# Kernel tuning notes

Measured on AMD Instinct MI355X. Metric: run time of the kernel, lower is better.

Reference implementation:

```python
import jax, jax.numpy as jnp
import numpy as np

B, S, HLEN, VLEN, HID = 32, 2048, 1024, 1024, 1024


def setup_inputs() -> dict:
    key = jax.random.key(0)
    ks = jax.random.split(key, 6)
    scale_W = 1.0 / np.sqrt(HLEN)
    scale_U = 1.0 / np.sqrt(VLEN)
    scale_w = 1.0 / np.sqrt(HID)
    return {
        "h": jax.random.normal(ks[0], (B, HLEN), dtype=jnp.float32),
        "V": jax.random.normal(ks[1], (B, S, VLEN), dtype=jnp.float32),
        "W_w": jax.random.normal(ks[2], (HID, HLEN), dtype=jnp.float32) * scale_W,
        "W_b": jax.random.normal(ks[3], (HID,), dtype=jnp.float32) * scale_W,
        "U_w": jax.random.normal(ks[4], (HID, VLEN), dtype=jnp.float32) * scale_U,
        "w_w": jax.random.normal(ks[5], (HID,), dtype=jnp.float32) * scale_w,
    }


def reference(h, V, W_w, W_b, U_w, w_w):
    # e = w^T tanh(W h + U V^T + b); beta = softmax(e); out = sum_s beta_s V_s
    h_proj = h @ W_w.T + W_b                      # [B, HID]
    V_proj = jnp.einsum('bsv,dv->bsd', V, U_w)    # [B, S, HID]
    e = jnp.einsum('bsd,d->bs', jnp.tanh(h_proj[:, None, :] + V_proj), w_w)  # [B, S]
    beta = jax.nn.softmax(e, axis=1)              # [B, S]
    return jnp.einsum('bs,bsv->bv', beta, V)      # [B, VLEN]
```

## Files before the change

### kernel.cpp

```cpp
#include <hip/hip_runtime.h>

constexpr int B_   = 32;
constexpr int S_   = 2048;
constexpr int HID_ = 1024;
constexpr int VL_  = 1024;

typedef __attribute__((ext_vector_type(4))) float  f32x4;
typedef __attribute__((ext_vector_type(4))) short  s16x4;
typedef __attribute__((ext_vector_type(8))) short  s16x8;

__device__ __forceinline__ short f2bf(float f) {
    union { float f; unsigned u; } v; v.f = f;
    unsigned r = v.u + 0x7fffu + ((v.u >> 16) & 1u);
    return (short)(r >> 16);
}

__device__ __forceinline__ float bf2f(short s) {
    union { unsigned u; float f; } v;
    v.u = ((unsigned)(unsigned short)s) << 16;
    return v.f;
}

__device__ __forceinline__ float fast_tanh(float x) {
    float e2 = __expf(2.0f * x);
    return 1.0f - 2.0f / (e2 + 1.0f);
}

__device__ __forceinline__ void async_cp16(const void* g, void* l) {
    __builtin_amdgcn_global_load_lds(
        (const __attribute__((address_space(1))) unsigned int*)g,
        (__attribute__((address_space(3))) unsigned int*)l,
        16, 0, 0);
}

__global__ __launch_bounds__(256) void hproj_kernel(const float* __restrict__ h,
                                                    const float* __restrict__ Ww,
                                                    const float* __restrict__ Wb,
                                                    float* __restrict__ hp) {
    int tid = threadIdx.x;
    int wave = tid >> 6, lane = tid & 63;
    int d = blockIdx.x * 4 + wave;
    const float* wr = Ww + (size_t)d * HID_;
    float4 wreg[4];
#pragma unroll
    for (int i = 0; i < 4; i++) wreg[i] = *(const float4*)(wr + i * 256 + lane * 4);
    float bias = Wb[d];
    for (int b = 0; b < B_; b++) {
        const float* hr = h + (size_t)b * HID_;
        float acc = 0.0f;
#pragma unroll
        for (int i = 0; i < 4; i++) {
            float4 x = *(const float4*)(hr + i * 256 + lane * 4);
            acc += wreg[i].x * x.x + wreg[i].y * x.y + wreg[i].z * x.z + wreg[i].w * x.w;
        }
#pragma unroll
        for (int o = 32; o; o >>= 1) acc += __shfl_xor(acc, o);
        if (lane == 0) hp[(size_t)b * HID_ + d] = acc + bias;
    }
}

__global__ __launch_bounds__(256) void cvt_kernel(const float* __restrict__ src,
                                                  short* __restrict__ dst, size_t n4) {
    size_t i = (size_t)blockIdx.x * blockDim.x + threadIdx.x;
    size_t stride = (size_t)gridDim.x * blockDim.x;
    for (; i < n4; i += stride) {
        float4 x = ((const float4*)src)[i];
        s16x4 y;
        y.x = f2bf(x.x); y.y = f2bf(x.y); y.z = f2bf(x.z); y.w = f2bf(x.w);
        ((s16x4*)dst)[i] = y;
    }
}

__global__ __launch_bounds__(256) void e_kernel_bf16(const short* __restrict__ Vm,
                                                     const short* __restrict__ Um,
                                                     const float* __restrict__ hp,
                                                     const float* __restrict__ ww,
                                                     float* __restrict__ epart) {
    __shared__ short As[128][32];
    __shared__ short Bs[128][32];
    __shared__ float ebuf[2][128];

    int tid = threadIdx.x;
    int dh = blockIdx.x;
    int s0 = blockIdx.y * 128;
    int b  = blockIdx.z;
    int wave = tid >> 6, lane = tid & 63;
    int wm = wave >> 1, wn = wave & 1;
    int col = lane & 15, quad = lane >> 4;

    int r0 = 32 * wave + (lane >> 2);
    int kc = (lane & 3) * 8;
    const short* gAb = Vm + ((size_t)b * S_ + s0 + r0) * VL_ + kc;
    short* lA0 = &As[32 * wave][0];
    short* lA1 = &As[32 * wave + 16][0];
    short* lB0 = &Bs[32 * wave][0];
    short* lB1 = &Bs[32 * wave + 16][0];

    float ep[4][4];
#pragma unroll
    for (int i = 0; i < 4; i++)
#pragma unroll
        for (int j = 0; j < 4; j++) ep[i][j] = 0.0f;

    for (int dt = dh * 4; dt < dh * 4 + 4; dt++) {
        int d0 = dt * 128;
        const short* gA0 = gAb;
        const short* gA1 = gAb + 16 * (size_t)VL_;
        const short* gB0 = Um + ((size_t)d0 + r0) * VL_ + kc;
        const short* gB1 = gB0 + 16 * (size_t)VL_;

        f32x4 zero = {0.f, 0.f, 0.f, 0.f};
        f32x4 acc[4][4];
#pragma unroll
        for (int i = 0; i < 4; i++)
#pragma unroll
            for (int j = 0; j < 4; j++) acc[i][j] = zero;

        for (int k0 = 0; k0 < VL_; k0 += 32) {
            async_cp16(gA0, lA0);
            async_cp16(gA1, lA1);
            async_cp16(gB0, lB0);
            async_cp16(gB1, lB1);
            gA0 += 32; gA1 += 32; gB0 += 32; gB1 += 32;
            __syncthreads();

            s16x8 a8[4], b8[4];
#pragma unroll
            for (int tm = 0; tm < 4; tm++)
                a8[tm] = *(const s16x8*)&As[wm * 64 + tm * 16 + col][quad * 8];
#pragma unroll
            for (int tn = 0; tn < 4; tn++)
                b8[tn] = *(const s16x8*)&Bs[wn * 64 + tn * 16 + col][quad * 8];
#pragma unroll
            for (int tm = 0; tm < 4; tm++)
#pragma unroll
                for (int tn = 0; tn < 4; tn++)
                    acc[tm][tn] = __builtin_amdgcn_mfma_f32_16x16x32_bf16(
                        a8[tm], b8[tn], acc[tm][tn], 0, 0, 0);
            __syncthreads();
        }

        float wv[4], hv[4];
#pragma unroll
        for (int tn = 0; tn < 4; tn++) {
            int d = d0 + wn * 64 + tn * 16 + col;
            wv[tn] = ww[d];
            hv[tn] = hp[(size_t)b * HID_ + d];
        }
#pragma unroll
        for (int tm = 0; tm < 4; tm++)
#pragma unroll
            for (int reg = 0; reg < 4; reg++) {
#pragma unroll
                for (int tn = 0; tn < 4; tn++)
                    ep[tm][reg] += wv[tn] * fast_tanh(hv[tn] + acc[tm][tn][reg]);
            }
    }

#pragma unroll
    for (int tm = 0; tm < 4; tm++)
#pragma unroll
        for (int reg = 0; reg < 4; reg++) {
            float p = ep[tm][reg];
            p += __shfl_xor(p, 1);
            p += __shfl_xor(p, 2);
            p += __shfl_xor(p, 4);
            p += __shfl_xor(p, 8);
            if (col == 0)
                ebuf[wn][wm * 64 + tm * 16 + quad * 4 + reg] = p;
        }
    __syncthreads();
    if (tid < 128)
        epart[((size_t)dh * B_ + b) * S_ + s0 + tid] = ebuf[0][tid] + ebuf[1][tid];
}

__global__ __launch_bounds__(256) void e_kernel_f32(const float* __restrict__ Vm,
                                                    const float* __restrict__ Um,
                                                    const float* __restrict__ hp,
                                                    const float* __restrict__ ww,
                                                    float* __restrict__ e) {
    __shared__ short As[128][40];
    __shared__ short Bs[128][40];
    int tid = threadIdx.x;
    int b  = blockIdx.z;
    int d0 = blockIdx.x * 128;
    int s0 = blockIdx.y * 128;
    int wave = tid >> 6, lane = tid & 63;
    int wm = wave >> 1, wn = wave & 1;
    int col = lane & 15, quad = lane >> 4;

    f32x4 zero = {0.f, 0.f, 0.f, 0.f};
    f32x4 acc[4][4];
#pragma unroll
    for (int i = 0; i < 4; i++)
#pragma unroll
        for (int j = 0; j < 4; j++) acc[i][j] = zero;

    const float* Abase = Vm + ((size_t)b * S_ + s0) * (size_t)VL_;
    const float* Bbase = Um + (size_t)d0 * (size_t)VL_;

    for (int k0 = 0; k0 < VL_; k0 += 32) {
        int k4 = tid & 7, rb = tid >> 3;
#pragma unroll
        for (int i = 0; i < 4; i++) {
            int r = rb + 32 * i;
            float4 x = *(const float4*)(Abase + (size_t)r * VL_ + k0 + k4 * 4);
            s16x4 ya; ya.x = f2bf(x.x); ya.y = f2bf(x.y); ya.z = f2bf(x.z); ya.w = f2bf(x.w);
            *(s16x4*)&As[r][k4 * 4] = ya;
            float4 y = *(const float4*)(Bbase + (size_t)r * VL_ + k0 + k4 * 4);
            s16x4 yb; yb.x = f2bf(y.x); yb.y = f2bf(y.y); yb.z = f2bf(y.z); yb.w = f2bf(y.w);
            *(s16x4*)&Bs[r][k4 * 4] = yb;
        }
        __syncthreads();
        s16x8 a8[4], b8[4];
#pragma unroll
        for (int tm = 0; tm < 4; tm++)
            a8[tm] = *(const s16x8*)&As[wm * 64 + tm * 16 + col][quad * 8];
#pragma unroll
        for (int tn = 0; tn < 4; tn++)
            b8[tn] = *(const s16x8*)&Bs[wn * 64 + tn * 16 + col][quad * 8];
#pragma unroll
        for (int tm = 0; tm < 4; tm++)
#pragma unroll
            for (int tn = 0; tn < 4; tn++)
                acc[tm][tn] = __builtin_amdgcn_mfma_f32_16x16x32_bf16(
                    a8[tm], b8[tn], acc[tm][tn], 0, 0, 0);
        __syncthreads();
    }

    float wv[4], hv[4];
#pragma unroll
    for (int tn = 0; tn < 4; tn++) {
        int d = d0 + wn * 64 + tn * 16 + col;
        wv[tn] = ww[d];
        hv[tn] = hp[(size_t)b * HID_ + d];
    }
#pragma unroll
    for (int tm = 0; tm < 4; tm++) {
#pragma unroll
        for (int reg = 0; reg < 4; reg++) {
            float p = 0.0f;
#pragma unroll
            for (int tn = 0; tn < 4; tn++)
                p += wv[tn] * fast_tanh(hv[tn] + acc[tm][tn][reg]);
            p += __shfl_xor(p, 1);
            p += __shfl_xor(p, 2);
            p += __shfl_xor(p, 4);
            p += __shfl_xor(p, 8);
            if (col == 0) {
                int s = s0 + wm * 64 + tm * 16 + quad * 4 + reg;
                atomicAdd(&e[(size_t)b * S_ + s], p);
            }
        }
    }
}

__global__ __launch_bounds__(256) void softmax_kernel(const float* __restrict__ epart,
                                                      float* __restrict__ beta,
                                                      int nparts) {
    int b = blockIdx.x, tid = threadIdx.x;
    const float* r0 = epart + (size_t)b * S_;
    const float* r1 = epart + ((size_t)B_ + b) * S_;
    float v[8];
    float m = -1e30f;
#pragma unroll
    for (int i = 0; i < 8; i++) {
        int idx = tid + i * 256;
        v[i] = r0[idx] + (nparts > 1 ? r1[idx] : 0.0f);
        m = fmaxf(m, v[i]);
    }
#pragma unroll
    for (int o = 32; o; o >>= 1) m = fmaxf(m, __shfl_xor(m, o));
    __shared__ float rm[4], rs[4];
    int wave = tid >> 6, lane = tid & 63;
    if (lane == 0) rm[wave] = m;
    __syncthreads();
    m = fmaxf(fmaxf(rm[0], rm[1]), fmaxf(rm[2], rm[3]));
    float s = 0.0f;
#pragma unroll
    for (int i = 0; i < 8; i++) { v[i] = __expf(v[i] - m); s += v[i]; }
#pragma unroll
    for (int o = 32; o; o >>= 1) s += __shfl_xor(s, o);
    if (lane == 0) rs[wave] = s;
    __syncthreads();
    s = rs[0] + rs[1] + rs[2] + rs[3];
    float inv = 1.0f / s;
#pragma unroll
    for (int i = 0; i < 8; i++) beta[(size_t)b * S_ + tid + i * 256] = v[i] * inv;
}

__global__ __launch_bounds__(256) void out_kernel_bf16(const float* __restrict__ beta,
                                                       const short* __restrict__ Vb16,
                                                       float* __restrict__ opart) {
    int b = blockIdx.x, sc = blockIdx.y;
    int v4 = threadIdx.x;
    const short* Vp = Vb16 + ((size_t)b * S_ + (size_t)sc * 128) * VL_;
    const float* bb = beta + (size_t)b * S_ + (size_t)sc * 128;
    float ax = 0.f, ay = 0.f, az = 0.f, aw = 0.f;
    for (int s = 0; s < 128; s++) {
        float w = bb[s];
        s16x4 x = *(const s16x4*)(Vp + (size_t)s * VL_ + v4 * 4);
        ax += w * bf2f(x.x); ay += w * bf2f(x.y);
        az += w * bf2f(x.z); aw += w * bf2f(x.w);
    }
    float4 r = {ax, ay, az, aw};
    *(float4*)(opart + (((size_t)b * 16 + sc) * VL_) + v4 * 4) = r;
}

__global__ __launch_bounds__(256) void out_reduce_kernel(const float* __restrict__ opart,
                                                         float* __restrict__ out) {
    int b = blockIdx.x, v4 = threadIdx.x;
    float4 a = {0.f, 0.f, 0.f, 0.f};
    const float* base = opart + (size_t)b * 16 * VL_;
#pragma unroll
    for (int sc = 0; sc < 16; sc++) {
        float4 x = *(const float4*)(base + (size_t)sc * VL_ + v4 * 4);
        a.x += x.x; a.y += x.y; a.z += x.z; a.w += x.w;
    }
    *(float4*)(out + (size_t)b * VL_ + v4 * 4) = a;
}

__global__ __launch_bounds__(256) void out_kernel_f32(const float* __restrict__ beta,
                                                      const float* __restrict__ V,
                                                      float* __restrict__ out) {
    int b = blockIdx.x, sc = blockIdx.y;
    int v4 = threadIdx.x;
    const float* Vb = V + ((size_t)b * S_ + (size_t)sc * 128) * VL_;
    const float* bb = beta + (size_t)b * S_ + (size_t)sc * 128;
    float ax = 0.f, ay = 0.f, az = 0.f, aw = 0.f;
    for (int s = 0; s < 128; s++) {
        float w = bb[s];
        float4 x = *(const float4*)(Vb + (size_t)s * VL_ + v4 * 4);
        ax += w * x.x; ay += w * x.y; az += w * x.z; aw += w * x.w;
    }
    float* o = out + (size_t)b * VL_ + v4 * 4;
    atomicAdd(o + 0, ax);
    atomicAdd(o + 1, ay);
    atomicAdd(o + 2, az);
    atomicAdd(o + 3, aw);
}

extern "C" void kernel_launch(void* const* d_in, const int* in_sizes, int n_in,
                              void* d_out, int out_size, void* d_ws, size_t ws_size,
                              hipStream_t stream) {
    const float* h  = (const float*)d_in[0];
    const float* V  = (const float*)d_in[1];
    const float* Ww = (const float*)d_in[2];
    const float* Wb = (const float*)d_in[3];
    const float* Uw = (const float*)d_in[4];
    const float* ww = (const float*)d_in[5];
    float* out = (float*)d_out;

    char* ws = (char*)d_ws;
    float* hp    = (float*)ws;
    float* epart = (float*)(ws + 131072);
    float* beta  = (float*)(ws + 131072 + 524288);
    float* opart = (float*)(ws + 131072 + 524288 + 262144);
    size_t fixed = 131072 + 524288 + 262144 + 2097152;
    short* Vb16 = (short*)(ws + fixed);
    short* Ub16 = Vb16 + (size_t)B_ * S_ * VL_;
    size_t need = fixed + ((size_t)B_ * S_ * VL_ + (size_t)HID_ * VL_) * 2;
    bool bf16path = (ws_size >= need);

    hproj_kernel<<<dim3(HID_ / 4), 256, 0, stream>>>(h, Ww, Wb, hp);

    if (bf16path) {
        cvt_kernel<<<4096, 256, 0, stream>>>(V, Vb16, (size_t)B_ * S_ * VL_ / 4);
        cvt_kernel<<<256, 256, 0, stream>>>(Uw, Ub16, (size_t)HID_ * VL_ / 4);
        e_kernel_bf16<<<dim3(2, S_ / 128, B_), 256, 0, stream>>>(Vb16, Ub16, hp, ww, epart);
        softmax_kernel<<<B_, 256, 0, stream>>>(epart, beta, 2);
        out_kernel_bf16<<<dim3(B_, S_ / 128), 256, 0, stream>>>(beta, Vb16, opart);
        out_reduce_kernel<<<B_, 256, 0, stream>>>(opart, out);
    } else {
        hipMemsetAsync(epart, 0, (size_t)B_ * S_ * 4, stream);
        hipMemsetAsync(out, 0, (size_t)out_size * 4, stream);
        e_kernel_f32<<<dim3(HID_ / 128, S_ / 128, B_), 256, 0, stream>>>(
            V, Uw, hp, ww, epart);
        softmax_kernel<<<B_, 256, 0, stream>>>(epart, beta, 1);
        out_kernel_f32<<<dim3(B_, S_ / 128), 256, 0, stream>>>(beta, V, out);
    }
}
```

Measured before the change: 663.9 us.

## Split bf16 e-kernel over eight HID tiles with swizzled 64-wide K staging

Each bf16 e-kernel block now handles one 128-wide HID tile instead of looping over four, so the grid grows to 8 HID tiles and softmax sums 8 partial e rows. K tiles grow from 32 to 64 with an XOR-swizzled shared-memory layout to avoid bank conflicts, which halves the number of barrier pairs, and the launch bound asks for 4 blocks per CU. The costs are re-reading the V tile 8 times instead of 2 and a larger epart workspace, which raises the bf16 path's workspace requirement.

```diff
diff --git a/kernel.cpp b/kernel.cpp
--- a/kernel.cpp
+++ b/kernel.cpp
@@ -71,97 +71,91 @@
     }
 }
 
-__global__ __launch_bounds__(256) void e_kernel_bf16(const short* __restrict__ Vm,
-                                                     const short* __restrict__ Um,
-                                                     const float* __restrict__ hp,
-                                                     const float* __restrict__ ww,
-                                                     float* __restrict__ epart) {
-    __shared__ short As[128][32];
-    __shared__ short Bs[128][32];
+__global__ __launch_bounds__(256, 4) void e_kernel_bf16(const short* __restrict__ Vm,
+                                                        const short* __restrict__ Um,
+                                                        const float* __restrict__ hp,
+                                                        const float* __restrict__ ww,
+                                                        float* __restrict__ epart) {
+    __shared__ short As[128 * 64];
+    __shared__ short Bs[128 * 64];
     __shared__ float ebuf[2][128];
 
     int tid = threadIdx.x;
-    int dh = blockIdx.x;
+    int dt = blockIdx.x;
     int s0 = blockIdx.y * 128;
     int b  = blockIdx.z;
     int wave = tid >> 6, lane = tid & 63;
     int wm = wave >> 1, wn = wave & 1;
     int col = lane & 15, quad = lane >> 4;
 
-    int r0 = 32 * wave + (lane >> 2);
-    int kc = (lane & 3) * 8;
-    const short* gAb = Vm + ((size_t)b * S_ + s0 + r0) * VL_ + kc;
-    short* lA0 = &As[32 * wave][0];
-    short* lA1 = &As[32 * wave + 16][0];
-    short* lB0 = &Bs[32 * wave][0];
-    short* lB1 = &Bs[32 * wave + 16][0];
-
-    float ep[4][4];
+    f32x4 acc[4][4];
 #pragma unroll
     for (int i = 0; i < 4; i++)
 #pragma unroll
-        for (int j = 0; j < 4; j++) ep[i][j] = 0.0f;
-
-    for (int dt = dh * 4; dt < dh * 4 + 4; dt++) {
-        int d0 = dt * 128;
-        const short* gA0 = gAb;
-        const short* gA1 = gAb + 16 * (size_t)VL_;
-        const short* gB0 = Um + ((size_t)d0 + r0) * VL_ + kc;
-        const short* gB1 = gB0 + 16 * (size_t)VL_;
-
-        f32x4 zero = {0.f, 0.f, 0.f, 0.f};
-        f32x4 acc[4][4];
-#pragma unroll
-        for (int i = 0; i < 4; i++)
-#pragma unroll
-            for (int j = 0; j < 4; j++) acc[i][j] = zero;
-
-        for (int k0 = 0; k0 < VL_; k0 += 32) {
-            async_cp16(gA0, lA0);
-            async_cp16(gA1, lA1);
-            async_cp16(gB0, lB0);
-            async_cp16(gB1, lB1);
-            gA0 += 32; gA1 += 32; gB0 += 32; gB1 += 32;
-            __syncthreads();
-
+        for (int j = 0; j < 4; j++) acc[i][j] = (f32x4){0.f, 0.f, 0.f, 0.f};
+
+    const short* Abase = Vm + ((size_t)b * S_ + s0) * VL_;
+    const short* Bbase = Um + (size_t)dt * 128 * VL_;
+    ptrdiff_t dBA = Bbase - Abase;
+    const short* srcA[4];
+    int il = lane >> 3, xl = lane & 7;
+#pragma unroll
+    for (int t = 0; t < 4; t++) {
+        int row = 32 * wave + 8 * t + il;
+        int kc8 = xl ^ ((row >> 1) & 7);
+        srcA[t] = Abase + (size_t)row * VL_ + kc8 * 8;
+    }
+
+    for (int it = 0; it < 16; it++) {
+#pragma unroll
+        for (int t = 0; t < 4; t++) {
+            async_cp16(srcA[t],       As + wave * 2048 + t * 512);
+            async_cp16(srcA[t] + dBA, Bs + wave * 2048 + t * 512);
+            srcA[t] += 64;
+        }
+        __syncthreads();
+
+#pragma unroll
+        for (int j = 0; j < 2; j++) {
             s16x8 a8[4], b8[4];
 #pragma unroll
-            for (int tm = 0; tm < 4; tm++)
-                a8[tm] = *(const s16x8*)&As[wm * 64 + tm * 16 + col][quad * 8];
-#pragma unroll
-            for (int tn = 0; tn < 4; tn++)
-                b8[tn] = *(const s16x8*)&Bs[wn * 64 + tn * 16 + col][quad * 8];
+            for (int tm = 0; tm < 4; tm++) {
+                int row = wm * 64 + tm * 16 + col;
+                int sl = row * 8 + ((j * 4 + quad) ^ ((row >> 1) & 7));
+                a8[tm] = *(const s16x8*)(As + sl * 8);
+            }
+#pragma unroll
+            for (int tn = 0; tn < 4; tn++) {
+                int row = wn * 64 + tn * 16 + col;
+                int sl = row * 8 + ((j * 4 + quad) ^ ((row >> 1) & 7));
+                b8[tn] = *(const s16x8*)(Bs + sl * 8);
+            }
 #pragma unroll
             for (int tm = 0; tm < 4; tm++)
 #pragma unroll
                 for (int tn = 0; tn < 4; tn++)
                     acc[tm][tn] = __builtin_amdgcn_mfma_f32_16x16x32_bf16(
                         a8[tm], b8[tn], acc[tm][tn], 0, 0, 0);
-            __syncthreads();
-        }
-
-        float wv[4], hv[4];
-#pragma unroll
-        for (int tn = 0; tn < 4; tn++) {
-            int d = d0 + wn * 64 + tn * 16 + col;
-            wv[tn] = ww[d];
-            hv[tn] = hp[(size_t)b * HID_ + d];
-        }
-#pragma unroll
-        for (int tm = 0; tm < 4; tm++)
-#pragma unroll
-            for (int reg = 0; reg < 4; reg++) {
-#pragma unroll
-                for (int tn = 0; tn < 4; tn++)
-                    ep[tm][reg] += wv[tn] * fast_tanh(hv[tn] + acc[tm][tn][reg]);
-            }
-    }
-
+        }
+        __syncthreads();
+    }
+
+    int d0 = dt * 128;
+    float wv[4], hv[4];
+#pragma unroll
+    for (int tn = 0; tn < 4; tn++) {
+        int d = d0 + wn * 64 + tn * 16 + col;
+        wv[tn] = ww[d];
+        hv[tn] = hp[(size_t)b * HID_ + d];
+    }
 #pragma unroll
     for (int tm = 0; tm < 4; tm++)
 #pragma unroll
         for (int reg = 0; reg < 4; reg++) {
-            float p = ep[tm][reg];
+            float p = 0.0f;
+#pragma unroll
+            for (int tn = 0; tn < 4; tn++)
+                p += wv[tn] * fast_tanh(hv[tn] + acc[tm][tn][reg]);
             p += __shfl_xor(p, 1);
             p += __shfl_xor(p, 2);
             p += __shfl_xor(p, 4);
@@ -171,7 +165,7 @@
         }
     __syncthreads();
     if (tid < 128)
-        epart[((size_t)dh * B_ + b) * S_ + s0 + tid] = ebuf[0][tid] + ebuf[1][tid];
+        epart[((size_t)dt * B_ + b) * S_ + s0 + tid] = ebuf[0][tid] + ebuf[1][tid];
 }
 
 __global__ __launch_bounds__(256) void e_kernel_f32(const float* __restrict__ Vm,
@@ -189,12 +183,11 @@
     int wm = wave >> 1, wn = wave & 1;
     int col = lane & 15, quad = lane >> 4;
 
-    f32x4 zero = {0.f, 0.f, 0.f, 0.f};
     f32x4 acc[4][4];
 #pragma unroll
     for (int i = 0; i < 4; i++)
 #pragma unroll
-        for (int j = 0; j < 4; j++) acc[i][j] = zero;
+        for (int j = 0; j < 4; j++) acc[i][j] = (f32x4){0.f, 0.f, 0.f, 0.f};
 
     const float* Abase = Vm + ((size_t)b * S_ + s0) * (size_t)VL_;
     const float* Bbase = Um + (size_t)d0 * (size_t)VL_;
@@ -259,14 +252,15 @@
                                                       float* __restrict__ beta,
                                                       int nparts) {
     int b = blockIdx.x, tid = threadIdx.x;
-    const float* r0 = epart + (size_t)b * S_;
-    const float* r1 = epart + ((size_t)B_ + b) * S_;
     float v[8];
     float m = -1e30f;
 #pragma unroll
     for (int i = 0; i < 8; i++) {
         int idx = tid + i * 256;
-        v[i] = r0[idx] + (nparts > 1 ? r1[idx] : 0.0f);
+        float s = 0.0f;
+        for (int p = 0; p < nparts; p++)
+            s += epart[((size_t)p * B_ + b) * S_ + idx];
+        v[i] = s;
         m = fmaxf(m, v[i]);
     }
 #pragma unroll
@@ -354,9 +348,9 @@
     char* ws = (char*)d_ws;
     float* hp    = (float*)ws;
     float* epart = (float*)(ws + 131072);
-    float* beta  = (float*)(ws + 131072 + 524288);
-    float* opart = (float*)(ws + 131072 + 524288 + 262144);
-    size_t fixed = 131072 + 524288 + 262144 + 2097152;
+    float* beta  = (float*)(ws + 131072 + 2097152);
+    float* opart = (float*)(ws + 131072 + 2097152 + 262144);
+    size_t fixed = 131072 + 2097152 + 262144 + 2097152;
     short* Vb16 = (short*)(ws + fixed);
     short* Ub16 = Vb16 + (size_t)B_ * S_ * VL_;
     size_t need = fixed + ((size_t)B_ * S_ * VL_ + (size_t)HID_ * VL_) * 2;
@@ -367,8 +361,8 @@
     if (bf16path) {
         cvt_kernel<<<4096, 256, 0, stream>>>(V, Vb16, (size_t)B_ * S_ * VL_ / 4);
         cvt_kernel<<<256, 256, 0, stream>>>(Uw, Ub16, (size_t)HID_ * VL_ / 4);
-        e_kernel_bf16<<<dim3(2, S_ / 128, B_), 256, 0, stream>>>(Vb16, Ub16, hp, ww, epart);
-        softmax_kernel<<<B_, 256, 0, stream>>>(epart, beta, 2);
+        e_kernel_bf16<<<dim3(8, S_ / 128, B_), 256, 0, stream>>>(Vb16, Ub16, hp, ww, epart);
+        softmax_kernel<<<B_, 256, 0, stream>>>(epart, beta, 8);
         out_kernel_bf16<<<dim3(B_, S_ / 128), 256, 0, stream>>>(beta, Vb16, opart);
         out_reduce_kernel<<<B_, 256, 0, stream>>>(opart, out);
     } else {
```

Result: no change. 670.4 us (+1.0%).
